# Optimization experiments

Measured on AMD Instinct MI355X. Metric: run time of the kernel, lower is better.

Reference implementation:

```python
import jax, jax.numpy as jnp
import numpy as np


def setup_inputs() -> dict:
    key = jax.random.key(0)
    ks = jax.random.split(key, 4)
    B, T, D, U = 256, 4096, 3, 8
    d = D + 1                      # time-augmented path dimension
    sig_dim = 1 + d + d * d        # depth-2 signature incl. constant term = 21
    glorot = jax.nn.initializers.glorot_uniform()
    return {
        "inputs": jax.random.normal(ks[0], (B, T, D), jnp.float32),
        "input_kernel": glorot(ks[1], (D, 3 * U), jnp.float32),
        "recurrent_kernel": glorot(ks[2], (U, 3 * U), jnp.float32),
        "forget_kernel": glorot(ks[3], (sig_dim, U), jnp.float32),
        "bias": jnp.zeros((4 * U,), jnp.float32),
    }


def _streamed_signature_depth2(path):
    """Streamed (cumulative) truncated signature of depth 2 via Chen's identity.
    path: (B, T, d) -> (B, T, 1 + d + d*d). Entry t is the signature of path[:t+1]."""
    B, T, d = path.shape
    dx = jnp.diff(path, axis=1)                                   # (B, T-1, d)
    L1 = jnp.cumsum(dx, axis=1)                                   # level-1
    L1_prev = jnp.concatenate([jnp.zeros((B, 1, d), path.dtype), L1[:, :-1]], axis=1)
    # Chen: L2_t = L2_{t-1} + L1_{t-1} (x) dx_t + 0.5 dx_t (x) dx_t
    terms = L1_prev[..., :, None] * dx[..., None, :] + 0.5 * dx[..., :, None] * dx[..., None, :]
    L2 = jnp.cumsum(terms, axis=1).reshape(B, T - 1, d * d)       # level-2
    sig = jnp.concatenate([jnp.ones((B, T - 1, 1), path.dtype), L1, L2], axis=-1)
    sig0 = jnp.concatenate(
        [jnp.ones((B, 1, 1), path.dtype), jnp.zeros((B, 1, d + d * d), path.dtype)], axis=-1)
    return jnp.concatenate([sig0, sig], axis=1)                   # (B, T, sig_dim)


def reference(inputs, input_kernel, recurrent_kernel, forget_kernel, bias):
    B, T, D = inputs.shape
    U = recurrent_kernel.shape[0]
    t_grid = jnp.linspace(0.0, 1.0, T)
    path = jnp.concatenate(
        [jnp.broadcast_to(t_grid[None, :, None], (B, T, 1)), inputs], axis=-1)
    sig = _streamed_signature_depth2(path)                        # (B, T, sig_dim)
    # normalize signatures at times t>0 by elapsed time (as in the original)
    sig = sig.at[:, 1:, :].set(sig[:, 1:, :] / t_grid[1:, None])

    b_i, b_f, b_c, b_o = jnp.split(bias, 4)
    x_proj = jnp.einsum('btd,du->btu', inputs, input_kernel)      # (B, T, 3U)

    def step(carry, xs):
        h, c = carry
        x_t, sig_t = xs
        gates = h @ recurrent_kernel + x_t                        # (B, 3U)
        i_t, c_hat, o_t = jnp.split(gates, 3, axis=-1)
        f_t = jax.nn.sigmoid(sig_t @ forget_kernel + b_f)         # signature forget gate
        i_t = jax.nn.sigmoid(i_t + b_i)
        c_hat = jnp.tanh(c_hat + b_c)
        o_t = jax.nn.sigmoid(o_t + b_o)
        c_new = f_t * c + i_t * c_hat
        h_new = o_t * jnp.tanh(c_new)
        return (h_new, c_new), h_new

    h0 = jnp.zeros((B, U), inputs.dtype)
    (_, _), h_seq = jax.lax.scan(
        step, (h0, h0), (x_proj.transpose(1, 0, 2), sig.transpose(1, 0, 2)))
    return h_seq.transpose(1, 0, 2)                               # (B, T, U)
```

## Files before the change

### kernel.cpp

```cpp
#include <hip/hip_runtime.h>
#include <hip/hip_bf16.h>

#define TT 4096
#define BB 256
#define DD 3
#define UU 8

#if defined(__has_builtin)
#if __has_builtin(__builtin_amdgcn_exp2f) && __has_builtin(__builtin_amdgcn_rcpf)
#define FAST_EXP2(x) __builtin_amdgcn_exp2f(x)
#define FAST_RCP(x)  __builtin_amdgcn_rcpf(x)
#endif
#endif
#ifndef FAST_EXP2
#define FAST_EXP2(x) exp2f(x)
#define FAST_RCP(x)  (1.0f / (x))
#endif

#define KI (-1.4426950408889634f)
#define KC (2.8853900817779268f)

__device__ __forceinline__ float fsig(float x) {
    float e = FAST_EXP2(KI * x);
    return FAST_RCP(1.0f + e);
}
__device__ __forceinline__ float ftanh(float x) {
    float e = FAST_EXP2(KC * x);
    return 1.0f - 2.0f * FAST_RCP(1.0f + e);
}

template <int CTRL>
__device__ __forceinline__ float dpp_f(float v) {
    int i = __builtin_bit_cast(int, v);
    i = __builtin_amdgcn_update_dpp(0, i, CTRL, 0xF, 0xF, true);
    return __builtin_bit_cast(float, i);
}

__device__ __forceinline__ float block_excl_scan(float v, int tid, float* red) {
    float x = v;
    int lid = tid & 63;
    #pragma unroll
    for (int d = 1; d < 64; d <<= 1) {
        float y = __shfl_up(x, d, 64);
        if (lid >= d) x += y;
    }
    int wave = tid >> 6;
    __syncthreads();
    if (lid == 63) red[wave] = x;
    __syncthreads();
    float off = 0.0f;
    for (int w = 0; w < wave; ++w) off += red[w];
    return off + (x - v);
}

__global__ __launch_bounds__(256) void sig_pre_kernel(
    const float* __restrict__ x,
    const float* __restrict__ Wi,
    const float* __restrict__ Wf,
    const float* __restrict__ bias,
    float* __restrict__ ws)
{
    __shared__ float sWf[21 * 8];
    __shared__ float sWi[3 * 24];
    __shared__ float sB[32];
    __shared__ float red[4];

    const int tid = threadIdx.x;
    const int b = blockIdx.x;
    if (tid < 168) sWf[tid] = Wf[tid];
    if (tid < 72)  sWi[tid] = Wi[tid];
    if (tid < 32)  sB[tid]  = bias[tid];
    __syncthreads();

    const float dtc = 1.0f / 4095.0f;
    const int t0 = tid * 16;
    const float* xb = x + (size_t)b * TT * DD;

    float l1[4] = {0.f, 0.f, 0.f, 0.f};
    float l2[16];
    #pragma unroll
    for (int i = 0; i < 16; ++i) l2[i] = 0.f;
    {
        int s = (tid == 0) ? 1 : t0;
        float xp0 = xb[(s - 1) * 3 + 0];
        float xp1 = xb[(s - 1) * 3 + 1];
        float xp2 = xb[(s - 1) * 3 + 2];
        for (; s < t0 + 16; ++s) {
            float c0 = xb[s * 3 + 0], c1 = xb[s * 3 + 1], c2 = xb[s * 3 + 2];
            float dxv[4] = {dtc, c0 - xp0, c1 - xp1, c2 - xp2};
            #pragma unroll
            for (int r = 0; r < 4; ++r) {
                float tr = l1[r] + 0.5f * dxv[r];
                #pragma unroll
                for (int cc = 0; cc < 4; ++cc)
                    l2[r * 4 + cc] = fmaf(tr, dxv[cc], l2[r * 4 + cc]);
            }
            #pragma unroll
            for (int r = 0; r < 4; ++r) l1[r] += dxv[r];
            xp0 = c0; xp1 = c1; xp2 = c2;
        }
    }

    float S1[4], O1[4];
    #pragma unroll
    for (int r = 0; r < 4; ++r) { S1[r] = l1[r]; }
    for (int r = 0; r < 4; ++r) O1[r] = block_excl_scan(S1[r], tid, red);
    float O2[16];
    for (int rc = 0; rc < 16; ++rc) {
        float c2v = l2[rc] + O1[rc >> 2] * S1[rc & 3];
        O2[rc] = block_excl_scan(c2v, tid, red);
    }

    #pragma unroll
    for (int r = 0; r < 4; ++r) l1[r] = O1[r];
    #pragma unroll
    for (int i = 0; i < 16; ++i) l2[i] = O2[i];

    float xp0, xp1, xp2;
    {
        int tp = (tid == 0) ? 0 : (t0 - 1);
        xp0 = xb[tp * 3 + 0]; xp1 = xb[tp * 3 + 1]; xp2 = xb[tp * 3 + 2];
    }
    for (int i2 = 0; i2 < 16; ++i2) {
        const int t = t0 + i2;
        float c0 = xb[t * 3 + 0], c1 = xb[t * 3 + 1], c2 = xb[t * 3 + 2];
        if (t > 0) {
            float dxv[4] = {dtc, c0 - xp0, c1 - xp1, c2 - xp2};
            #pragma unroll
            for (int r = 0; r < 4; ++r) {
                float tr = l1[r] + 0.5f * dxv[r];
                #pragma unroll
                for (int cc = 0; cc < 4; ++cc)
                    l2[r * 4 + cc] = fmaf(tr, dxv[cc], l2[r * 4 + cc]);
            }
            #pragma unroll
            for (int r = 0; r < 4; ++r) l1[r] += dxv[r];
        }
        xp0 = c0; xp1 = c1; xp2 = c2;
        const float scale = (t == 0) ? 1.0f : (4095.0f / (float)t);
        float sg[21];
        sg[0] = scale;
        #pragma unroll
        for (int r = 0; r < 4; ++r) sg[1 + r] = l1[r] * scale;
        #pragma unroll
        for (int rc = 0; rc < 16; ++rc) sg[5 + rc] = l2[rc] * scale;

        float fa[8];
        #pragma unroll
        for (int u = 0; u < 8; ++u) fa[u] = sB[8 + u];
        #pragma unroll
        for (int j = 0; j < 21; ++j) {
            float s = sg[j];
            #pragma unroll
            for (int u = 0; u < 8; ++u) fa[u] = fmaf(s, sWf[j * 8 + u], fa[u]);
        }
        float g[24];
        #pragma unroll
        for (int u = 0; u < 8; ++u) {
            g[u] = sB[u]; g[8 + u] = sB[16 + u]; g[16 + u] = sB[24 + u];
        }
        #pragma unroll
        for (int gg = 0; gg < 24; ++gg) {
            g[gg] = fmaf(c0, sWi[gg], g[gg]);
            g[gg] = fmaf(c1, sWi[24 + gg], g[gg]);
            g[gg] = fmaf(c2, sWi[48 + gg], g[gg]);
        }
        float4* wp = (float4*)ws + ((size_t)t * BB + b) * UU;
        #pragma unroll
        for (int u = 0; u < 8; ++u)
            wp[u] = make_float4(KI * g[u], KC * g[8 + u], KI * g[16 + u], fsig(fa[u]));
    }
}

#define RING 16
__global__ __launch_bounds__(64) void lstm_scan_full(
    const float* __restrict__ ws, const float* __restrict__ Wr,
    float* __restrict__ out)
{
    const int lane = threadIdx.x;
    const int u = lane & 7;
    const int b = blockIdx.x * 8 + (lane >> 3);
    float wa[8], wb[8], wc[8];
    #pragma unroll
    for (int m = 0; m < 8; ++m) {
        int j = u ^ m;
        wa[m] = KI * Wr[j * 24 + u];
        wb[m] = KC * Wr[j * 24 + 8 + u];
        wc[m] = KI * Wr[j * 24 + 16 + u];
    }
    const float4* gp = (const float4*)ws + (size_t)b * 8 + u;
    float4 buf[RING];
    #pragma unroll
    for (int p = 0; p < RING; ++p) buf[p] = gp[(size_t)p * (BB * UU)];
    float h = 0.f, c = 0.f;
    float* op = out + (size_t)b * TT * 8 + u;

    auto step = [&](int t, float4 g) {
        float h7 = dpp_f<0x141>(h);
        float h1 = dpp_f<0xB1>(h);
        float h2 = dpp_f<0x4E>(h);
        float h3 = dpp_f<0x1B>(h);
        float h6 = dpp_f<0xB1>(h7);
        float h5 = dpp_f<0x4E>(h7);
        float h4 = dpp_f<0x1B>(h7);
        float gi = fmaf(h, wa[0], g.x), giB = h7 * wa[7];
        float gc = fmaf(h, wb[0], g.y), gcB = h7 * wb[7];
        float go = fmaf(h, wc[0], g.z), goB = h7 * wc[7];
        gi = fmaf(h1, wa[1], gi);  giB = fmaf(h6, wa[6], giB);
        gc = fmaf(h1, wb[1], gc);  gcB = fmaf(h6, wb[6], gcB);
        go = fmaf(h1, wc[1], go);  goB = fmaf(h6, wc[6], goB);
        gi = fmaf(h2, wa[2], gi);  giB = fmaf(h5, wa[5], giB);
        gc = fmaf(h2, wb[2], gc);  gcB = fmaf(h5, wb[5], gcB);
        go = fmaf(h2, wc[2], go);  goB = fmaf(h5, wc[5], goB);
        gi = fmaf(h3, wa[3], gi);  giB = fmaf(h4, wa[4], giB);
        gc = fmaf(h3, wb[3], gc);  gcB = fmaf(h4, wb[4], gcB);
        go = fmaf(h3, wc[3], go);  goB = fmaf(h4, wc[4], goB);
        gi += giB; gc += gcB; go += goB;
        float iv  = FAST_RCP(1.0f + FAST_EXP2(gi));
        float rcv = FAST_RCP(1.0f + FAST_EXP2(gc));
        float ov  = FAST_RCP(1.0f + FAST_EXP2(go));
        float cv2 = fmaf(-2.0f * KC, rcv, KC);
        c = fmaf(g.w, c, iv * cv2);
        float rc = FAST_RCP(1.0f + FAST_EXP2(c));
        float m2ov = -2.0f * ov;
        h = fmaf(m2ov, rc, ov);
        op[(size_t)t * 8] = h;
    };

    for (int tb = 0; tb + RING < TT; tb += RING) {
        #pragma unroll
        for (int j = 0; j < RING; ++j) {
            const int t = tb + j;
            float4 g = buf[j];
            buf[j] = gp[(size_t)(t + RING) * (BB * UU)];
            step(t, g);
        }
    }
    #pragma unroll
    for (int j = 0; j < RING; ++j) step(TT - RING + j, buf[j]);
}

__global__ __launch_bounds__(64) void lstm_scan_ultra(
    const float* __restrict__ x, const float* __restrict__ Wi,
    const float* __restrict__ Wr, const float* __restrict__ Wf,
    const float* __restrict__ bias, float* __restrict__ out)
{
    const int lane = threadIdx.x;
    const int u = lane & 7;
    const int q = lane >> 3;
    const int b = blockIdx.x * 8 + q;
    float wa[8], wb[8], wc[8];
    #pragma unroll
    for (int m = 0; m < 8; ++m) {
        int j = u ^ m;
        wa[m] = Wr[j * 24 + u];
        wb[m] = Wr[j * 24 + 8 + u];
        wc[m] = Wr[j * 24 + 16 + u];
    }
    float wia[3], wib[3], wic[3];
    #pragma unroll
    for (int k = 0; k < 3; ++k) {
        wia[k] = Wi[k * 24 + u];
        wib[k] = Wi[k * 24 + 8 + u];
        wic[k] = Wi[k * 24 + 16 + u];
    }
    float wf[21];
    #pragma unroll
    for (int j = 0; j < 21; ++j) wf[j] = Wf[j * 8 + u];
    const float bi = bias[u], bf = bias[8 + u], bc = bias[16 + u], bo = bias[24 + u];
    const float* xb = x + (size_t)b * TT * 3;
    float l1[4] = {0.f, 0.f, 0.f, 0.f};
    float l2[16];
    #pragma unroll
    for (int i = 0; i < 16; ++i) l2[i] = 0.f;
    float xp0 = xb[0], xp1 = xb[1], xp2 = xb[2];
    float h = 0.f, c = 0.f;
    float* op = out + (size_t)b * TT * 8 + u;
    const float dtc = 1.0f / 4095.0f;
    for (int t = 0; t < TT; ++t) {
        float c0 = xb[t * 3 + 0], c1 = xb[t * 3 + 1], c2 = xb[t * 3 + 2];
        if (t > 0) {
            float dxv[4] = {dtc, c0 - xp0, c1 - xp1, c2 - xp2};
            #pragma unroll
            for (int r = 0; r < 4; ++r) {
                float tr = l1[r] + 0.5f * dxv[r];
                #pragma unroll
                for (int cc = 0; cc < 4; ++cc)
                    l2[r * 4 + cc] = fmaf(tr, dxv[cc], l2[r * 4 + cc]);
            }
            #pragma unroll
            for (int r = 0; r < 4; ++r) l1[r] += dxv[r];
        }
        xp0 = c0; xp1 = c1; xp2 = c2;
        const float scale = (t == 0) ? 1.0f : (4095.0f / (float)t);
        float dot = wf[0];
        #pragma unroll
        for (int r = 0; r < 4; ++r) dot = fmaf(l1[r], wf[1 + r], dot);
        #pragma unroll
        for (int rc = 0; rc < 16; ++rc) dot = fmaf(l2[rc], wf[5 + rc], dot);
        float fv = fsig(fmaf(scale, dot, bf));
        float gi = bi, gc = bc, go = bo;
        gi = fmaf(c0, wia[0], gi); gi = fmaf(c1, wia[1], gi); gi = fmaf(c2, wia[2], gi);
        gc = fmaf(c0, wib[0], gc); gc = fmaf(c1, wib[1], gc); gc = fmaf(c2, wib[2], gc);
        go = fmaf(c0, wic[0], go); go = fmaf(c1, wic[1], go); go = fmaf(c2, wic[2], go);
        float h1 = dpp_f<0xB1>(h);
        float h2 = dpp_f<0x4E>(h);
        float h3 = dpp_f<0x1B>(h);
        float h7 = dpp_f<0x141>(h);
        float h6 = dpp_f<0xB1>(h7);
        float h5 = dpp_f<0x4E>(h7);
        float h4 = dpp_f<0x1B>(h7);
        gi = fmaf(h, wa[0], gi); gi = fmaf(h1, wa[1], gi); gi = fmaf(h2, wa[2], gi); gi = fmaf(h3, wa[3], gi);
        gi = fmaf(h4, wa[4], gi); gi = fmaf(h5, wa[5], gi); gi = fmaf(h6, wa[6], gi); gi = fmaf(h7, wa[7], gi);
        gc = fmaf(h, wb[0], gc); gc = fmaf(h1, wb[1], gc); gc = fmaf(h2, wb[2], gc); gc = fmaf(h3, wb[3], gc);
        gc = fmaf(h4, wb[4], gc); gc = fmaf(h5, wb[5], gc); gc = fmaf(h6, wb[6], gc); gc = fmaf(h7, wb[7], gc);
        go = fmaf(h, wc[0], go); go = fmaf(h1, wc[1], go); go = fmaf(h2, wc[2], go); go = fmaf(h3, wc[3], go);
        go = fmaf(h4, wc[4], go); go = fmaf(h5, wc[5], go); go = fmaf(h6, wc[6], go); go = fmaf(h7, wc[7], go);
        float iv = fsig(gi);
        float cv = ftanh(gc);
        float ov = fsig(go);
        c = fmaf(fv, c, iv * cv);
        h = ov * ftanh(c);
        op[(size_t)t * 8] = h;
    }
}

extern "C" void kernel_launch(void* const* d_in, const int* in_sizes, int n_in,
                              void* d_out, int out_size, void* d_ws, size_t ws_size,
                              hipStream_t stream) {
    const float* x    = (const float*)d_in[0];
    const float* Wi   = (const float*)d_in[1];
    const float* Wr   = (const float*)d_in[2];
    const float* Wf   = (const float*)d_in[3];
    const float* bias = (const float*)d_in[4];
    float* out = (float*)d_out;

    const size_t need = (size_t)TT * BB * UU * 4 * sizeof(float);
    if (ws_size >= need) {
        sig_pre_kernel<<<dim3(BB), dim3(256), 0, stream>>>(x, Wi, Wf, bias, (float*)d_ws);
        lstm_scan_full<<<dim3(BB / 8), dim3(64), 0, stream>>>((const float*)d_ws, Wr, out);
    } else {
        lstm_scan_ultra<<<dim3(BB / 8), dim3(64), 0, stream>>>(x, Wi, Wr, Wf, bias, out);
    }
}
```

Before: 677.4 us.

## Spread LSTM gates across lanes so each wave processes two batch rows

The recurrent scan now gives each gate (input, candidate, output, forget) its own group of 8 lanes, with 2 batch rows per 64-lane wave and 128 blocks instead of 32. Each lane does one 8-term dot product and one transcendental per step instead of three, which shortens the serial per-step dependency chain. Gates are combined with a DPP exchange and cross-half shuffles. The precompute kernel now writes a gate-major workspace layout, and the forget sigmoid moves into the scan. This costs extra cross-lane traffic and one more exp/rcp per step for the forget gate.

Result: slower. 789.4 us (+16.5%).

```diff
diff --git a/kernel.cpp b/kernel.cpp
--- a/kernel.cpp
+++ b/kernel.cpp
@@ -34,6 +34,10 @@
     int i = __builtin_bit_cast(int, v);
     i = __builtin_amdgcn_update_dpp(0, i, CTRL, 0xF, 0xF, true);
     return __builtin_bit_cast(float, i);
+}
+
+__device__ __forceinline__ float xswap_sum(float v) {
+    return v + __shfl_xor(v, 32, 64);
 }
 
 __device__ __forceinline__ float block_excl_scan(float v, int tid, float* red) {
@@ -165,37 +169,58 @@
             g[gg] = fmaf(c1, sWi[24 + gg], g[gg]);
             g[gg] = fmaf(c2, sWi[48 + gg], g[gg]);
         }
-        float4* wp = (float4*)ws + ((size_t)t * BB + b) * UU;
-        #pragma unroll
-        for (int u = 0; u < 8; ++u)
-            wp[u] = make_float4(KI * g[u], KC * g[8 + u], KI * g[16 + u], fsig(fa[u]));
-    }
-}
-
-#define RING 16
-__global__ __launch_bounds__(64) void lstm_scan_full(
+        float4* wp = (float4*)(ws + ((size_t)t * BB + b) * 32);
+        wp[0] = make_float4(KI * g[0],  KI * g[1],  KI * g[2],  KI * g[3]);
+        wp[1] = make_float4(KI * g[4],  KI * g[5],  KI * g[6],  KI * g[7]);
+        wp[2] = make_float4(KC * g[8],  KC * g[9],  KC * g[10], KC * g[11]);
+        wp[3] = make_float4(KC * g[12], KC * g[13], KC * g[14], KC * g[15]);
+        wp[4] = make_float4(KI * g[16], KI * g[17], KI * g[18], KI * g[19]);
+        wp[5] = make_float4(KI * g[20], KI * g[21], KI * g[22], KI * g[23]);
+        wp[6] = make_float4(KI * fa[0], KI * fa[1], KI * fa[2], KI * fa[3]);
+        wp[7] = make_float4(KI * fa[4], KI * fa[5], KI * fa[6], KI * fa[7]);
+    }
+}
+
+#define RING 8
+__global__ __launch_bounds__(64) void lstm_scan_wide(
     const float* __restrict__ ws, const float* __restrict__ Wr,
     float* __restrict__ out)
 {
     const int lane = threadIdx.x;
-    const int u = lane & 7;
-    const int b = blockIdx.x * 8 + (lane >> 3);
-    float wa[8], wb[8], wc[8];
-    #pragma unroll
-    for (int m = 0; m < 8; ++m) {
-        int j = u ^ m;
-        wa[m] = KI * Wr[j * 24 + u];
-        wb[m] = KC * Wr[j * 24 + 8 + u];
-        wc[m] = KI * Wr[j * 24 + 16 + u];
-    }
-    const float4* gp = (const float4*)ws + (size_t)b * 8 + u;
-    float4 buf[RING];
-    #pragma unroll
-    for (int p = 0; p < RING; ++p) buf[p] = gp[(size_t)p * (BB * UU)];
-    float h = 0.f, c = 0.f;
+    const int u  = lane & 7;
+    const int gl = (lane >> 3) & 1;
+    const int q  = (lane >> 4) & 1;
+    const int gh = (lane >> 5) & 1;
+    const int g  = gh * 2 + gl;
+    const int b  = blockIdx.x * 2 + q;
+    const bool isC = (g == 1);
+    const bool b3 = (gl != 0);
+    const bool hiH = (gh != 0);
+    const bool do_store = (g == 0);
+
+    float wv[8];
+    #pragma unroll
+    for (int m = 0; m < 8; ++m) wv[m] = 0.0f;
+    if (g != 3) {
+        const float sc = isC ? KC : KI;
+        #pragma unroll
+        for (int m = 0; m < 8; ++m)
+            wv[m] = sc * Wr[(u ^ m) * 24 + g * 8 + u];
+    }
+    const float Aact = isC ? (-2.0f * KC) : 1.0f;
+    const float Bact = isC ? KC : 0.0f;
+
+    const int comp = ((lane & 32) >> 1) | (lane & 15);
+    const float* gp = ws + (size_t)b * 32 + comp;
     float* op = out + (size_t)b * TT * 8 + u;
 
-    auto step = [&](int t, float4 g) {
+    float buf[RING];
+    #pragma unroll
+    for (int p = 0; p < RING; ++p) buf[p] = gp[(size_t)p * (BB * 32)];
+
+    float h = 0.0f, cs = 0.0f;
+
+    auto step = [&](int t, float pre) {
         float h7 = dpp_f<0x141>(h);
         float h1 = dpp_f<0xB1>(h);
         float h2 = dpp_f<0x4E>(h);
@@ -203,37 +228,34 @@
         float h6 = dpp_f<0xB1>(h7);
         float h5 = dpp_f<0x4E>(h7);
         float h4 = dpp_f<0x1B>(h7);
-        float gi = fmaf(h, wa[0], g.x), giB = h7 * wa[7];
-        float gc = fmaf(h, wb[0], g.y), gcB = h7 * wb[7];
-        float go = fmaf(h, wc[0], g.z), goB = h7 * wc[7];
-        gi = fmaf(h1, wa[1], gi);  giB = fmaf(h6, wa[6], giB);
-        gc = fmaf(h1, wb[1], gc);  gcB = fmaf(h6, wb[6], gcB);
-        go = fmaf(h1, wc[1], go);  goB = fmaf(h6, wc[6], goB);
-        gi = fmaf(h2, wa[2], gi);  giB = fmaf(h5, wa[5], giB);
-        gc = fmaf(h2, wb[2], gc);  gcB = fmaf(h5, wb[5], gcB);
-        go = fmaf(h2, wc[2], go);  goB = fmaf(h5, wc[5], goB);
-        gi = fmaf(h3, wa[3], gi);  giB = fmaf(h4, wa[4], giB);
-        gc = fmaf(h3, wb[3], gc);  gcB = fmaf(h4, wb[4], gcB);
-        go = fmaf(h3, wc[3], go);  goB = fmaf(h4, wc[4], goB);
-        gi += giB; gc += gcB; go += goB;
-        float iv  = FAST_RCP(1.0f + FAST_EXP2(gi));
-        float rcv = FAST_RCP(1.0f + FAST_EXP2(gc));
-        float ov  = FAST_RCP(1.0f + FAST_EXP2(go));
-        float cv2 = fmaf(-2.0f * KC, rcv, KC);
-        c = fmaf(g.w, c, iv * cv2);
-        float rc = FAST_RCP(1.0f + FAST_EXP2(c));
-        float m2ov = -2.0f * ov;
-        h = fmaf(m2ov, rc, ov);
-        op[(size_t)t * 8] = h;
+        float a0 = fmaf(h,  wv[0], pre), a1 = h7 * wv[7];
+        a0 = fmaf(h1, wv[1], a0); a1 = fmaf(h6, wv[6], a1);
+        a0 = fmaf(h2, wv[2], a0); a1 = fmaf(h5, wv[5], a1);
+        a0 = fmaf(h3, wv[3], a0); a1 = fmaf(h4, wv[4], a1);
+        float acc = a0 + a1;
+        float r = FAST_RCP(1.0f + FAST_EXP2(acc));
+        float act = fmaf(Aact, r, Bact);
+        float x8 = dpp_f<0x128>(act);
+        float prod  = act * x8;
+        float fsel  = b3 ? act : x8;
+        float ovsel = b3 ? x8  : act;
+        float w = fsel * cs;
+        float send  = hiH ? w : prod;
+        float osend = hiH ? ovsel : 0.0f;
+        cs = xswap_sum(send);
+        float o1 = xswap_sum(osend);
+        float r2 = FAST_RCP(1.0f + FAST_EXP2(cs));
+        h = fmaf(-2.0f * o1, r2, o1);
+        if (do_store) op[(size_t)t * 8] = h;
     };
 
     for (int tb = 0; tb + RING < TT; tb += RING) {
         #pragma unroll
         for (int j = 0; j < RING; ++j) {
             const int t = tb + j;
-            float4 g = buf[j];
-            buf[j] = gp[(size_t)(t + RING) * (BB * UU)];
-            step(t, g);
+            float pre = buf[j];
+            buf[j] = gp[(size_t)(t + RING) * (BB * 32)];
+            step(t, pre);
         }
     }
     #pragma unroll
@@ -335,10 +357,10 @@
     const float* bias = (const float*)d_in[4];
     float* out = (float*)d_out;
 
-    const size_t need = (size_t)TT * BB * UU * 4 * sizeof(float);
+    const size_t need = (size_t)TT * BB * 32 * sizeof(float);
     if (ws_size >= need) {
         sig_pre_kernel<<<dim3(BB), dim3(256), 0, stream>>>(x, Wi, Wf, bias, (float*)d_ws);
-        lstm_scan_full<<<dim3(BB / 8), dim3(64), 0, stream>>>((const float*)d_ws, Wr, out);
+        lstm_scan_wide<<<dim3(BB / 2), dim3(64), 0, stream>>>((const float*)d_ws, Wr, out);
     } else {
         lstm_scan_ultra<<<dim3(BB / 8), dim3(64), 0, stream>>>(x, Wi, Wr, Wf, bias, out);
     }
```

## Split gate work across two lane rows and interleave two batch chains per wave

Applied to the files above, without the earlier changes.

Restructures the recurrent scan so each batch element uses 16 lanes instead of 8. One 8-lane half computes the input and candidate gates, the other computes the output and forget gates, and they exchange activations through a DPP row shift. Each wave now carries two independent batch recurrences that are interleaved to hide latency. The precompute kernel writes a matching float2-pair layout, and the forget-gate sigmoid moves into the scan. This cuts the serial FMA chain per lane from 24 to 16. It adds one extra transcendental, DPP exchanges and selects to each step, and halves the register ring depth.

Measured after the change: 1.036 ms. 53.0% more time.

```diff
diff --git a/kernel.cpp b/kernel.cpp
--- a/kernel.cpp
+++ b/kernel.cpp
@@ -165,79 +165,113 @@
             g[gg] = fmaf(c1, sWi[24 + gg], g[gg]);
             g[gg] = fmaf(c2, sWi[48 + gg], g[gg]);
         }
-        float4* wp = (float4*)ws + ((size_t)t * BB + b) * UU;
-        #pragma unroll
-        for (int u = 0; u < 8; ++u)
-            wp[u] = make_float4(KI * g[u], KC * g[8 + u], KI * g[16 + u], fsig(fa[u]));
-    }
-}
-
-#define RING 16
-__global__ __launch_bounds__(64) void lstm_scan_full(
+        float4* wp = (float4*)(ws + ((size_t)t * BB + b) * 32);
+        #pragma unroll
+        for (int k = 0; k < 4; ++k) {
+            wp[k] = make_float4(KI * g[2 * k],     KI * g[16 + 2 * k],
+                                KI * g[2 * k + 1], KI * g[16 + 2 * k + 1]);
+            wp[4 + k] = make_float4(KC * g[8 + 2 * k],     KI * fa[2 * k],
+                                    KC * g[8 + 2 * k + 1], KI * fa[2 * k + 1]);
+        }
+    }
+}
+
+#define RING 8
+#define TSTRIDE (BB * 16)
+__global__ __launch_bounds__(64) void lstm_scan_row16(
     const float* __restrict__ ws, const float* __restrict__ Wr,
     float* __restrict__ out)
 {
     const int lane = threadIdx.x;
     const int u = lane & 7;
-    const int b = blockIdx.x * 8 + (lane >> 3);
-    float wa[8], wb[8], wc[8];
+    const bool hiR = (lane & 8) != 0;
+    const int q = lane >> 4;
+    const int b0 = blockIdx.x * 8 + q;
+    const int b1 = b0 + 4;
+
+    float wvA[8], wvB[8];
     #pragma unroll
     for (int m = 0; m < 8; ++m) {
         int j = u ^ m;
-        wa[m] = KI * Wr[j * 24 + u];
-        wb[m] = KC * Wr[j * 24 + 8 + u];
-        wc[m] = KI * Wr[j * 24 + 16 + u];
-    }
-    const float4* gp = (const float4*)ws + (size_t)b * 8 + u;
-    float4 buf[RING];
-    #pragma unroll
-    for (int p = 0; p < RING; ++p) buf[p] = gp[(size_t)p * (BB * UU)];
-    float h = 0.f, c = 0.f;
-    float* op = out + (size_t)b * TT * 8 + u;
-
-    auto step = [&](int t, float4 g) {
-        float h7 = dpp_f<0x141>(h);
-        float h1 = dpp_f<0xB1>(h);
-        float h2 = dpp_f<0x4E>(h);
-        float h3 = dpp_f<0x1B>(h);
-        float h6 = dpp_f<0xB1>(h7);
-        float h5 = dpp_f<0x4E>(h7);
-        float h4 = dpp_f<0x1B>(h7);
-        float gi = fmaf(h, wa[0], g.x), giB = h7 * wa[7];
-        float gc = fmaf(h, wb[0], g.y), gcB = h7 * wb[7];
-        float go = fmaf(h, wc[0], g.z), goB = h7 * wc[7];
-        gi = fmaf(h1, wa[1], gi);  giB = fmaf(h6, wa[6], giB);
-        gc = fmaf(h1, wb[1], gc);  gcB = fmaf(h6, wb[6], gcB);
-        go = fmaf(h1, wc[1], go);  goB = fmaf(h6, wc[6], goB);
-        gi = fmaf(h2, wa[2], gi);  giB = fmaf(h5, wa[5], giB);
-        gc = fmaf(h2, wb[2], gc);  gcB = fmaf(h5, wb[5], gcB);
-        go = fmaf(h2, wc[2], go);  goB = fmaf(h5, wc[5], goB);
-        gi = fmaf(h3, wa[3], gi);  giB = fmaf(h4, wa[4], giB);
-        gc = fmaf(h3, wb[3], gc);  gcB = fmaf(h4, wb[4], gcB);
-        go = fmaf(h3, wc[3], go);  goB = fmaf(h4, wc[4], goB);
-        gi += giB; gc += gcB; go += goB;
-        float iv  = FAST_RCP(1.0f + FAST_EXP2(gi));
-        float rcv = FAST_RCP(1.0f + FAST_EXP2(gc));
-        float ov  = FAST_RCP(1.0f + FAST_EXP2(go));
-        float cv2 = fmaf(-2.0f * KC, rcv, KC);
-        c = fmaf(g.w, c, iv * cv2);
-        float rc = FAST_RCP(1.0f + FAST_EXP2(c));
+        wvA[m] = hiR ? (KC * Wr[j * 24 + 8 + u]) : (KI * Wr[j * 24 + u]);
+        wvB[m] = hiR ? 0.0f : (KI * Wr[j * 24 + 16 + u]);
+    }
+    const float Aact = hiR ? (-2.0f * KC) : 1.0f;
+    const float Bact = hiR ? KC : 0.0f;
+
+    const float2* gp0 = (const float2*)ws + (size_t)b0 * 16 + (lane & 15);
+    const float2* gp1 = (const float2*)ws + (size_t)b1 * 16 + (lane & 15);
+    float* op0 = out + (size_t)b0 * TT * 8 + u;
+    float* op1 = out + (size_t)b1 * TT * 8 + u;
+
+    float2 buf0[RING], buf1[RING];
+    #pragma unroll
+    for (int p = 0; p < RING; ++p) {
+        buf0[p] = gp0[(size_t)p * TSTRIDE];
+        buf1[p] = gp1[(size_t)p * TSTRIDE];
+    }
+
+    float h0 = 0.f, cs0 = 0.f;
+    float h1 = 0.f, cs1 = 0.f;
+
+    auto step = [&](float& h, float& cs, float2 g) {
+        float r7 = dpp_f<0x141>(h);
+        float r1 = dpp_f<0xB1>(h);
+        float r2 = dpp_f<0x4E>(h);
+        float r3 = dpp_f<0x1B>(h);
+        float r6 = dpp_f<0xB1>(r7);
+        float r5 = dpp_f<0x4E>(r7);
+        float r4 = dpp_f<0x1B>(r7);
+        float a0 = fmaf(h,  wvA[0], g.x), a1 = r7 * wvA[7];
+        float b0_ = fmaf(h, wvB[0], g.y), b1_ = r7 * wvB[7];
+        a0 = fmaf(r1, wvA[1], a0);  a1 = fmaf(r6, wvA[6], a1);
+        b0_ = fmaf(r1, wvB[1], b0_); b1_ = fmaf(r6, wvB[6], b1_);
+        a0 = fmaf(r2, wvA[2], a0);  a1 = fmaf(r5, wvA[5], a1);
+        b0_ = fmaf(r2, wvB[2], b0_); b1_ = fmaf(r5, wvB[5], b1_);
+        a0 = fmaf(r3, wvA[3], a0);  a1 = fmaf(r4, wvA[4], a1);
+        b0_ = fmaf(r3, wvB[3], b0_); b1_ = fmaf(r4, wvB[4], b1_);
+        float accA = a0 + a1;
+        float accB = b0_ + b1_;
+        float rA = FAST_RCP(1.0f + FAST_EXP2(accA));
+        float rB = FAST_RCP(1.0f + FAST_EXP2(accB));
+        float actA = fmaf(Aact, rA, Bact);
+        float xA = dpp_f<0x128>(actA);
+        float xB = dpp_f<0x128>(rB);
+        float ivcv = actA * xA;
+        float fv = hiR ? rB : xB;
+        float ov = hiR ? xB : rB;
+        cs = fmaf(fv, cs, ivcv);
+        float rc = FAST_RCP(1.0f + FAST_EXP2(cs));
         float m2ov = -2.0f * ov;
         h = fmaf(m2ov, rc, ov);
-        op[(size_t)t * 8] = h;
     };
 
     for (int tb = 0; tb + RING < TT; tb += RING) {
         #pragma unroll
         for (int j = 0; j < RING; ++j) {
             const int t = tb + j;
-            float4 g = buf[j];
-            buf[j] = gp[(size_t)(t + RING) * (BB * UU)];
-            step(t, g);
-        }
-    }
-    #pragma unroll
-    for (int j = 0; j < RING; ++j) step(TT - RING + j, buf[j]);
+            float2 g0 = buf0[j];
+            float2 g1 = buf1[j];
+            buf0[j] = gp0[(size_t)(t + RING) * TSTRIDE];
+            buf1[j] = gp1[(size_t)(t + RING) * TSTRIDE];
+            step(h0, cs0, g0);
+            step(h1, cs1, g1);
+            if (!hiR) {
+                op0[(size_t)t * 8] = h0;
+                op1[(size_t)t * 8] = h1;
+            }
+        }
+    }
+    #pragma unroll
+    for (int j = 0; j < RING; ++j) {
+        const int t = TT - RING + j;
+        step(h0, cs0, buf0[j]);
+        step(h1, cs1, buf1[j]);
+        if (!hiR) {
+            op0[(size_t)t * 8] = h0;
+            op1[(size_t)t * 8] = h1;
+        }
+    }
 }
 
 __global__ __launch_bounds__(64) void lstm_scan_ultra(
@@ -335,10 +369,10 @@
     const float* bias = (const float*)d_in[4];
     float* out = (float*)d_out;
 
-    const size_t need = (size_t)TT * BB * UU * 4 * sizeof(float);
+    const size_t need = (size_t)TT * BB * 32 * sizeof(float);
     if (ws_size >= need) {
         sig_pre_kernel<<<dim3(BB), dim3(256), 0, stream>>>(x, Wi, Wf, bias, (float*)d_ws);
-        lstm_scan_full<<<dim3(BB / 8), dim3(64), 0, stream>>>((const float*)d_ws, Wr, out);
+        lstm_scan_row16<<<dim3(BB / 8), dim3(64), 0, stream>>>((const float*)d_ws, Wr, out);
     } else {
         lstm_scan_ultra<<<dim3(BB / 8), dim3(64), 0, stream>>>(x, Wi, Wr, Wf, bias, out);
     }
```
